# Kernel tuning notes

Hardware: AMD Instinct MI355X
Metric: run time of the kernel (lower is better)

## Reference

```python
import jax, jax.numpy as jnp
import numpy as np

D_MODEL = 256
D_INNER = 512          # expand * d_model
HEADDIM = 64
NHEADS = D_INNER // HEADDIM   # 8
NGROUPS = 1
D_STATE = 64
D_IN_PROJ = 2 * D_INNER + 2 * NGROUPS * D_STATE + NHEADS   # 1160
CONV_DIM = D_INNER + 2 * NGROUPS * D_STATE                  # 640
LN_EPS = 1e-5


def setup_inputs() -> dict:
    key = jax.random.key(0)
    ks = jax.random.split(key, 16)
    s = 0.02
    # dt_bias init as in torch code
    dt = jnp.exp(jax.random.uniform(ks[10], (NHEADS,)) * (np.log(0.1) - np.log(0.001)) + np.log(0.001))
    dt = jnp.clip(dt, 1e-4)
    dt_bias = dt + jnp.log(-jnp.expm1(-dt))
    A_log = jnp.log(jax.random.uniform(ks[11], (NHEADS,), minval=1.0, maxval=16.0))
    return {
        "u": jax.random.normal(ks[0], (4, 8192, D_MODEL), dtype=jnp.float32),
        "H": 64,
        "W": 128,
        "W_in": jax.random.normal(ks[1], (D_IN_PROJ, D_MODEL), dtype=jnp.float32) * s,
        "W_stereo": jax.random.normal(ks[2], (D_IN_PROJ, D_INNER), dtype=jnp.float32) * s,
        "conv_l_w": jax.random.normal(ks[3], (CONV_DIM, 1, 3, 3), dtype=jnp.float32) * 0.1,
        "conv_l_b": jax.random.normal(ks[4], (CONV_DIM,), dtype=jnp.float32) * 0.01,
        "conv_r_w": jax.random.normal(ks[5], (CONV_DIM, 1, 3, 3), dtype=jnp.float32) * 0.1,
        "conv_r_b": jax.random.normal(ks[6], (CONV_DIM,), dtype=jnp.float32) * 0.01,
        "conv_w": jax.random.normal(ks[7], (CONV_DIM, 1, 3, 3), dtype=jnp.float32) * 0.1,
        "conv_b": jax.random.normal(ks[8], (CONV_DIM,), dtype=jnp.float32) * 0.01,
        "dt_bias": dt_bias,
        "A_log": A_log,
        "D_l": jnp.ones((NHEADS,), dtype=jnp.float32),
        "D_r": jnp.ones((NHEADS,), dtype=jnp.float32),
        "D": jnp.ones((NHEADS,), dtype=jnp.float32),
        "ln_g": jnp.ones((D_INNER,), dtype=jnp.float32),
        "ln_b": jnp.zeros((D_INNER,), dtype=jnp.float32),
        "W_out": jax.random.normal(ks[9], (D_MODEL, D_INNER), dtype=jnp.float32) * s,
    }


def _dwconv(x, w, b):
    # x: (B, C, H, W); depthwise 3x3 conv, SAME padding ((d_conv-1)//2 = 1)
    y = jax.lax.conv_general_dilated(
        x, w, window_strides=(1, 1), padding='SAME',
        dimension_numbers=('NCHW', 'OIHW', 'NCHW'),
        feature_group_count=CONV_DIM)
    return y + b[None, :, None, None]


def _layernorm(x, g, b):
    mu = x.mean(-1, keepdims=True)
    var = x.var(-1, keepdims=True)
    return (x - mu) / jnp.sqrt(var + LN_EPS) * g + b


def _lin_attn(x, dt, A, Bm, Cm, Dp):
    # x: (b, l, d_inner), dt: (b, l, h), Bm/Cm: (b, l, d_state); ngroups == 1
    b, l, _ = x.shape
    xh = x.reshape(b, l, NHEADS, HEADDIM)              # V: (b, l, h, p)
    dA = -(dt[..., None] * A[None, None, :, None])     # ssd_positve_dA -> -dt*A, (b,l,h,1)
    KV = jnp.einsum('bls,blhp->bhsp', Bm, xh * dA)     # K^T @ V_scaled
    y = jnp.einsum('bls,bhsp->blhp', Cm, KV)           # Q @ KV
    y = y + xh * Dp[None, None, :, None]               # skip D
    return y.reshape(b, l, D_INNER)


def reference(u, H, W, W_in, W_stereo, conv_l_w, conv_l_b, conv_r_w, conv_r_b,
              conv_w, conv_b, dt_bias, A_log, D_l, D_r, D, ln_g, ln_b, W_out):
    batch, seqlen, _ = u.shape
    half = batch // 2
    silu = jax.nn.silu
    A = -jnp.exp(A_log)

    zxbcdt = u @ W_in.T                                             # (b, l, 1160)
    z, xBC, dt = jnp.split(zxbcdt, [D_INNER, D_INNER + CONV_DIM], axis=-1)
    dt = jax.nn.softplus(dt + dt_bias)                              # (b, l, h)

    xBC = xBC.reshape(batch, H, W, CONV_DIM).transpose(0, 3, 1, 2)  # NCHW
    xBC1 = silu(_dwconv(xBC[:half], conv_l_w, conv_l_b)).transpose(0, 2, 3, 1).reshape(half, H * W, CONV_DIM)
    xBC2 = silu(_dwconv(xBC[half:], conv_r_w, conv_r_b)).transpose(0, 2, 3, 1).reshape(half, H * W, CONV_DIM)

    x1, B1, C1 = jnp.split(xBC1, [D_INNER, D_INNER + NGROUPS * D_STATE], axis=-1)
    x2, B2, C2 = jnp.split(xBC2, [D_INNER, D_INNER + NGROUPS * D_STATE], axis=-1)
    dt1, dt2 = dt[:half], dt[half:]

    y1 = _layernorm(_lin_attn(x1, dt1, A, B1, C1, D_l), ln_g, ln_b)
    y2 = _layernorm(_lin_attn(x2, dt2, A, B2, C2, D_r), ln_g, ln_b)
    y = jnp.concatenate([y1, y2], axis=0) * z

    zxs = y @ W_stereo.T
    zs, xBCs, dts = jnp.split(zxs, [D_INNER, D_INNER + CONV_DIM], axis=-1)
    dts = jax.nn.softplus(dts + dt_bias)

    xBCs = xBCs.reshape(batch, H, W, CONV_DIM).transpose(0, 3, 1, 2)
    xBCs = silu(_dwconv(xBCs, conv_w, conv_b)).transpose(0, 2, 3, 1).reshape(batch, H * W, CONV_DIM)
    xs, Bs, Cs = jnp.split(xBCs, [D_INNER, D_INNER + NGROUPS * D_STATE], axis=-1)

    ys = _layernorm(_lin_attn(xs, dts, A, Bs, Cs, D), ln_g, ln_b) * zs
    return ys @ W_out.T
```

## Files before the change

### kernel.cpp

```cpp
#include <hip/hip_runtime.h>
#include <hip/hip_bf16.h>
#include <math.h>

#define NB    4
#define LSEQ  8192
#define HH    64
#define WW    128
#define DMODEL 256
#define DINNER 512
#define NH    8
#define DSTATE 64
#define DPROJ 1160
#define CONVD 640
#define MROWS (NB*LSEQ)
#define KVCH  32
#define CBLK  80

typedef unsigned short bf16_t;
typedef __attribute__((ext_vector_type(8))) unsigned short ushort8v;
typedef __attribute__((ext_vector_type(8))) short short8v;
typedef __attribute__((ext_vector_type(4))) float f32x4;

static __device__ __forceinline__ float bf2f(bf16_t u) {
    return __uint_as_float(((unsigned)u) << 16);
}
static __device__ __forceinline__ bf16_t f2bf(float f) {
    unsigned u = __float_as_uint(f);
    u += 0x7FFFu + ((u >> 16) & 1u);
    return (bf16_t)(u >> 16);
}

template <typename TC>
__global__ __launch_bounds__(256) void gemm_mfma_pipe(
    const bf16_t* __restrict__ A, int lda,
    const bf16_t* __restrict__ B, int ldb,
    TC* __restrict__ C, int ldc,
    int M, int N, int K)
{
    __shared__ __align__(16) bf16_t As[3][128 * 32];
    __shared__ __align__(16) bf16_t Bs[3][128 * 32];
    const int nwg = gridDim.x * gridDim.y;
    const int wg  = blockIdx.y * gridDim.x + blockIdx.x;
    const int swz = (wg & 7) * (nwg >> 3) + (wg >> 3);
    const int bx  = swz % gridDim.x;
    const int by  = swz / gridDim.x;

    const int tid = threadIdx.x;
    const int m0 = by * 128;
    const int n0 = bx * 128;
    const int wid = tid >> 6;
    const int lane = tid & 63;
    const int hA = wid >> 1;
    const int hB = wid & 1;
    const int fr = lane & 15;
    const int kq = lane >> 4;

    f32x4 acc[4][4];
    #pragma unroll
    for (int i = 0; i < 4; ++i)
        #pragma unroll
        for (int j = 0; j < 4; ++j) acc[i][j] = (f32x4){0.f, 0.f, 0.f, 0.f};

    int srow[2], scol[2];
    #pragma unroll
    for (int i = 0; i < 2; ++i) {
        const int L = i * 256 + tid;
        srow[i] = ((L >> 8) << 6) + (((L >> 6) & 3) << 4) + ((L >> 2) & 15);
        scol[i] = (L & 3) * 8;
    }

#define STAGE_P(buf, k0)                                                       \
    {                                                                          \
        _Pragma("unroll")                                                      \
        for (int i = 0; i < 2; ++i) {                                          \
            const size_t ga = (size_t)(m0 + srow[i]) * lda + (k0) + scol[i];   \
            const size_t gb = (size_t)(n0 + srow[i]) * ldb + (k0) + scol[i];   \
            const int ldst = (i * 256 + tid) * 8;                              \
            __builtin_amdgcn_global_load_lds(                                  \
                (const __attribute__((address_space(1))) void*)(A + ga),       \
                (__attribute__((address_space(3))) void*)(&As[buf][ldst]), 16, 0, 0); \
            __builtin_amdgcn_global_load_lds(                                  \
                (const __attribute__((address_space(1))) void*)(B + gb),       \
                (__attribute__((address_space(3))) void*)(&Bs[buf][ldst]), 16, 0, 0); \
        }                                                                      \
    }

    const int nt = K >> 5;
    STAGE_P(0, 0);
    STAGE_P(1, 32);

    const int abase = hA * 2048 + (fr * 4 + kq) * 8;
    const int bbase = hB * 2048 + (fr * 4 + kq) * 8;

    for (int t = 0; t < nt; ++t) {
        const int cur = t % 3;
        if (t + 1 < nt) asm volatile("s_waitcnt vmcnt(4)" ::: "memory");
        else            asm volatile("s_waitcnt vmcnt(0)" ::: "memory");
        __builtin_amdgcn_s_barrier();
        __builtin_amdgcn_sched_barrier(0);

        if (t + 2 < nt) STAGE_P((t + 2) % 3, (t + 2) * 32);

        short8v a_frag[4], b_frag[4];
        #pragma unroll
        for (int m = 0; m < 4; ++m)
            a_frag[m] = *(const short8v*)&As[cur][abase + m * 512];
        #pragma unroll
        for (int n = 0; n < 4; ++n)
            b_frag[n] = *(const short8v*)&Bs[cur][bbase + n * 512];
        #pragma unroll
        for (int m = 0; m < 4; ++m)
            #pragma unroll
            for (int n = 0; n < 4; ++n)
                acc[m][n] = __builtin_amdgcn_mfma_f32_16x16x32_bf16(
                    a_frag[m], b_frag[n], acc[m][n], 0, 0, 0);
    }
#undef STAGE_P

    const int wr = hA * 64;
    const int wc = hB * 64;
    #pragma unroll
    for (int mi = 0; mi < 4; ++mi) {
        #pragma unroll
        for (int ni = 0; ni < 4; ++ni) {
            const int col = n0 + wc + ni * 16 + fr;
            if (col < N) {
                #pragma unroll
                for (int q = 0; q < 4; ++q) {
                    const int row = m0 + wr + mi * 16 + kq * 4 + q;
                    if constexpr (sizeof(TC) == 2)
                        C[(size_t)row * ldc + col] = f2bf(acc[mi][ni][q]);
                    else
                        C[(size_t)row * ldc + col] = acc[mi][ni][q];
                }
            }
        }
    }
}

template <typename TC>
__global__ __launch_bounds__(256) void gemm_mfma_bt(
    const bf16_t* __restrict__ A, int lda, size_t sAb,
    const bf16_t* __restrict__ B, int ldb, size_t sBb,
    TC* __restrict__ C, int ldc, size_t sCb,
    int M, int N, int K)
{
    __shared__ __align__(16) bf16_t As[128 * 32];
    __shared__ __align__(16) bf16_t Bs[128 * 32];
    const bf16_t* Ab = A + blockIdx.z * sAb;
    const bf16_t* Bb = B + blockIdx.z * sBb;
    TC*            Cb = C + blockIdx.z * sCb;
    const int tid = threadIdx.x;
    const int m0 = blockIdx.y * 128;
    const int n0 = blockIdx.x * 128;
    const int wid = tid >> 6;
    const int lane = tid & 63;
    const int wr = (wid >> 1) * 64;
    const int wc = (wid & 1) * 64;
    const int fr = lane & 15;
    const int fk = (lane >> 4) * 8;

    f32x4 acc[4][4];
    #pragma unroll
    for (int i = 0; i < 4; ++i)
        #pragma unroll
        for (int j = 0; j < 4; ++j) acc[i][j] = (f32x4){0.f, 0.f, 0.f, 0.f};

    const int srow = tid >> 2;
    const int scol = (tid & 3) * 8;
    const bf16_t* gA = Ab + (size_t)(m0 + srow) * lda + scol;
    const bf16_t* gB = Bb + (size_t)(n0 + srow) * ldb + scol;
    bf16_t* lA = As + tid * 8;
    bf16_t* lB = Bs + tid * 8;

    for (int k0 = 0; k0 < K; k0 += 32) {
        __builtin_amdgcn_global_load_lds(
            (const __attribute__((address_space(1))) void*)(gA + k0),
            (__attribute__((address_space(3))) void*)lA, 16, 0, 0);
        __builtin_amdgcn_global_load_lds(
            (const __attribute__((address_space(1))) void*)(gA + (size_t)64 * lda + k0),
            (__attribute__((address_space(3))) void*)(lA + 2048), 16, 0, 0);
        __builtin_amdgcn_global_load_lds(
            (const __attribute__((address_space(1))) void*)(gB + k0),
            (__attribute__((address_space(3))) void*)lB, 16, 0, 0);
        __builtin_amdgcn_global_load_lds(
            (const __attribute__((address_space(1))) void*)(gB + (size_t)64 * ldb + k0),
            (__attribute__((address_space(3))) void*)(lB + 2048), 16, 0, 0);
        __syncthreads();

        short8v a_frag[4], b_frag[4];
        #pragma unroll
        for (int m = 0; m < 4; ++m)
            a_frag[m] = *(const short8v*)&As[(wr + m * 16 + fr) * 32 + fk];
        #pragma unroll
        for (int n = 0; n < 4; ++n)
            b_frag[n] = *(const short8v*)&Bs[(wc + n * 16 + fr) * 32 + fk];
        #pragma unroll
        for (int m = 0; m < 4; ++m)
            #pragma unroll
            for (int n = 0; n < 4; ++n)
                acc[m][n] = __builtin_amdgcn_mfma_f32_16x16x32_bf16(
                    a_frag[m], b_frag[n], acc[m][n], 0, 0, 0);
        __syncthreads();
    }

    #pragma unroll
    for (int mi = 0; mi < 4; ++mi) {
        #pragma unroll
        for (int ni = 0; ni < 4; ++ni) {
            const int col = n0 + wc + ni * 16 + fr;
            if (col < N) {
                #pragma unroll
                for (int q = 0; q < 4; ++q) {
                    const int row = m0 + wr + mi * 16 + (lane >> 4) * 4 + q;
                    if constexpr (sizeof(TC) == 2)
                        Cb[(size_t)row * ldc + col] = f2bf(acc[mi][ni][q]);
                    else
                        Cb[(size_t)row * ldc + col] = acc[mi][ni][q];
                }
            }
        }
    }
}

__global__ __launch_bounds__(256) void cvt_bf16_kernel(
    const float* __restrict__ in, bf16_t* __restrict__ out, int n)
{
    const int base = (blockIdx.x * 256 + threadIdx.x) * 4;
    if (base >= n) return;
    float4 v = *(const float4*)&in[base];
    ushort4 o;
    o.x = f2bf(v.x); o.y = f2bf(v.y); o.z = f2bf(v.z); o.w = f2bf(v.w);
    *(ushort4*)&out[base] = o;
}

__global__ __launch_bounds__(256) void wpad_kernel(
    const float* __restrict__ W, bf16_t* __restrict__ Wp,
    int N, int Npad, int K)
{
    const int i = blockIdx.x * 256 + threadIdx.x;
    if (i >= Npad * K) return;
    const int r = i / K, k = i - r * K;
    Wp[i] = (r < N) ? f2bf(W[(size_t)r * K + k]) : (bf16_t)0;
}

__global__ __launch_bounds__(256) void dt_kernel(
    const bf16_t* __restrict__ zx, const float* __restrict__ dt_bias,
    float* __restrict__ dtbuf)
{
    const int idx = blockIdx.x * 256 + threadIdx.x;
    const int h = idx & 7;
    const int row = idx >> 3;
    const float v = bf2f(zx[(size_t)row * DPROJ + (DINNER + CONVD) + h]) + dt_bias[h];
    const float sp = (v > 0.f) ? (v + log1pf(expf(-v))) : log1pf(expf(v));
    dtbuf[idx] = sp;
}

__global__ __launch_bounds__(256) void conv_silu_kernel(
    const bf16_t* __restrict__ zx,
    const float* __restrict__ wA, const float* __restrict__ bA,
    const float* __restrict__ wB, const float* __restrict__ bB,
    bf16_t* __restrict__ out)
{
    const int idx = blockIdx.x * 256 + threadIdx.x;
    const int cb = idx % CBLK;
    const int pc = idx / CBLK;
    const int c0 = cb * 8;
    const int ww = pc & (WW - 1);
    const int h4 = (pc >> 7) & 15;
    const int b  = pc >> 11;
    const int hbase = h4 * 4;
    const float* wp = (b < 2) ? wA : wB;
    const float* bp = (b < 2) ? bA : bB;

    float w[72];
    const float4* wsrc = (const float4*)(wp + c0 * 9);
    #pragma unroll
    for (int i = 0; i < 18; ++i) ((float4*)w)[i] = wsrc[i];

    float acc[4][8];
    {
        float4 bv0 = *(const float4*)(bp + c0);
        float4 bv1 = *(const float4*)(bp + c0 + 4);
        #pragma unroll
        for (int o = 0; o < 4; ++o) {
            acc[o][0] = bv0.x; acc[o][1] = bv0.y; acc[o][2] = bv0.z; acc[o][3] = bv0.w;
            acc[o][4] = bv1.x; acc[o][5] = bv1.y; acc[o][6] = bv1.z; acc[o][7] = bv1.w;
        }
    }

    const bf16_t* base = zx + (size_t)b * LSEQ * DPROJ + DINNER + c0;
    #pragma unroll
    for (int ri = 0; ri < 6; ++ri) {
        const int hi = hbase + ri - 1;
        const bool hok = (unsigned)hi < (unsigned)HH;
        float cur[3][8];
        #pragma unroll
        for (int kj = 0; kj < 3; ++kj) {
            const int wi = ww + kj - 1;
            if (hok && (unsigned)wi < (unsigned)WW) {
                const ushort8v v = *(const ushort8v*)(base + (size_t)(hi * WW + wi) * DPROJ);
                #pragma unroll
                for (int q = 0; q < 8; ++q) cur[kj][q] = bf2f(v[q]);
            } else {
                #pragma unroll
                for (int q = 0; q < 8; ++q) cur[kj][q] = 0.f;
            }
        }
        #pragma unroll
        for (int o = 0; o < 4; ++o) {
            const int ki = ri - o;
            if (ki >= 0 && ki < 3) {
                #pragma unroll
                for (int kj = 0; kj < 3; ++kj)
                    #pragma unroll
                    for (int q = 0; q < 8; ++q)
                        acc[o][q] += cur[kj][q] * w[q * 9 + ki * 3 + kj];
            }
        }
    }

    #pragma unroll
    for (int o = 0; o < 4; ++o) {
        const int t = b * LSEQ + (hbase + o) * WW + ww;
        ushort8v ov;
        #pragma unroll
        for (int q = 0; q < 8; ++q) {
            const float s = acc[o][q] / (1.f + expf(-acc[o][q]));
            ov[q] = f2bf(s);
        }
        *(ushort8v*)(out + (size_t)t * CONVD + c0) = ov;
    }
}

__global__ __launch_bounds__(128) void kv_part_kernel(
    const bf16_t* __restrict__ xconv, const float* __restrict__ dtbuf,
    const float* __restrict__ A_log, float* __restrict__ KVp)
{
    const int h = blockIdx.y, b = blockIdx.z, chunk = blockIdx.x;
    const int tid = threadIdx.x;
    const int w = tid >> 6, lane = tid & 63;
    __shared__ float lds[2 * 4352];
    float* Bt = lds + w * 4352;
    float* Xt = Bt + 2176;
    const float eA = expf(A_log[h]);
    const int s4  = (lane & 15) * 4;
    const int p16 = (lane >> 4) * 16;
    const int r    = lane & 31;
    const int part = lane >> 5;

    float acc[4][16];
    #pragma unroll
    for (int i = 0; i < 4; ++i)
        #pragma unroll
        for (int j = 0; j < 16; ++j) acc[i][j] = 0.f;

    const int l0 = b * LSEQ + chunk * 256;

    for (int t = 0; t < 8; t += 2) {
        const int row = l0 + (t + w) * 32 + r;
        const bf16_t* src = xconv + (size_t)row * CONVD + (part ? h * 64 : DINNER);
        const float scale = part ? dtbuf[row * NH + h] * eA : 1.f;
        float* dst = part ? &Xt[r * 68] : &Bt[r * 68];
        #pragma unroll
        for (int j = 0; j < 8; ++j) {
            ushort8v v = *(const ushort8v*)(src + j * 8);
            f32x4 lo = {bf2f(v[0]) * scale, bf2f(v[1]) * scale,
                        bf2f(v[2]) * scale, bf2f(v[3]) * scale};
            f32x4 hi = {bf2f(v[4]) * scale, bf2f(v[5]) * scale,
                        bf2f(v[6]) * scale, bf2f(v[7]) * scale};
            *(f32x4*)&dst[j * 8]     = lo;
            *(f32x4*)&dst[j * 8 + 4] = hi;
        }
        __syncthreads();
        #pragma unroll 4
        for (int rr = 0; rr < 32; ++rr) {
            const f32x4 bv = *(const f32x4*)&Bt[rr * 68 + s4];
            #pragma unroll
            for (int q = 0; q < 4; ++q) {
                const f32x4 xv = *(const f32x4*)&Xt[rr * 68 + p16 + q * 4];
                #pragma unroll
                for (int si = 0; si < 4; ++si)
                    #pragma unroll
                    for (int k = 0; k < 4; ++k)
                        acc[si][q * 4 + k] += bv[si] * xv[k];
            }
        }
        __syncthreads();
    }

    if (w == 0) {
        #pragma unroll
        for (int si = 0; si < 4; ++si)
            #pragma unroll
            for (int q = 0; q < 4; ++q)
                *(f32x4*)&lds[(s4 + si) * 68 + p16 + q * 4] =
                    (f32x4){acc[si][q*4], acc[si][q*4+1], acc[si][q*4+2], acc[si][q*4+3]};
    }
    __syncthreads();
    if (w == 1) {
        float* dst = KVp + ((size_t)chunk * (NB * NH) + (b * NH + h)) * 4096;
        #pragma unroll
        for (int si = 0; si < 4; ++si)
            #pragma unroll
            for (int q = 0; q < 4; ++q) {
                const f32x4 o = *(const f32x4*)&lds[(s4 + si) * 68 + p16 + q * 4];
                f32x4 v = {acc[si][q*4] + o[0], acc[si][q*4+1] + o[1],
                           acc[si][q*4+2] + o[2], acc[si][q*4+3] + o[3]};
                *(f32x4*)&dst[(s4 + si) * 64 + p16 + q * 4] = v;
            }
    }
}

__global__ __launch_bounds__(256) void kv_reduce_T_kernel(
    const float* __restrict__ KVp, bf16_t* __restrict__ KVT)
{
    const int idx = blockIdx.x * 256 + threadIdx.x;
    float s = 0.f;
    #pragma unroll
    for (int c = 0; c < KVCH; ++c) s += KVp[(size_t)c * 131072 + idx];
    const int bh = idx >> 12;
    const int ss = (idx >> 6) & 63;
    const int p  = idx & 63;
    KVT[((size_t)(bh * 64 + p)) * 64 + ss] = f2bf(s);
}

__global__ __launch_bounds__(256) void ln_gate_kernel(
    const bf16_t* __restrict__ Yattn, const bf16_t* __restrict__ xconv,
    const bf16_t* __restrict__ zx,
    const float* __restrict__ DA, const float* __restrict__ DB,
    const float* __restrict__ ln_g, const float* __restrict__ ln_b,
    bf16_t* __restrict__ ybuf)
{
    const int w = threadIdx.x >> 6, lane = threadIdx.x & 63;
    const int c0 = lane * 8;
    const int h = lane >> 3;
    float g[8], be[8];
    *(float4*)&g[0]  = *(const float4*)&ln_g[c0];
    *(float4*)&g[4]  = *(const float4*)&ln_g[c0 + 4];
    *(float4*)&be[0] = *(const float4*)&ln_b[c0];
    *(float4*)&be[4] = *(const float4*)&ln_b[c0 + 4];
    const int row0 = (blockIdx.x * 4 + w) * 4;

    for (int i = 0; i < 4; ++i) {
        const int row = row0 + i;
        const int b = row >> 13;
        const float Dv = (b < 2) ? DA[h] : DB[h];
        ushort8v yv = *(const ushort8v*)(Yattn + (size_t)row * DINNER + c0);
        ushort8v xv = *(const ushort8v*)(xconv + (size_t)row * CONVD + c0);
        float y[8];
        float s1 = 0.f, s2 = 0.f;
        #pragma unroll
        for (int q = 0; q < 8; ++q) {
            y[q] = bf2f(yv[q]) + bf2f(xv[q]) * Dv;
            s1 += y[q]; s2 += y[q] * y[q];
        }
        #pragma unroll
        for (int off = 32; off > 0; off >>= 1) {
            s1 += __shfl_xor(s1, off, 64);
            s2 += __shfl_xor(s2, off, 64);
        }
        const float mu = s1 * (1.f / 512.f);
        const float var = s2 * (1.f / 512.f) - mu * mu;
        const float rstd = rsqrtf(var + 1e-5f);
        ushort8v zv = *(const ushort8v*)(zx + (size_t)row * DPROJ + c0);
        ushort8v o;
        #pragma unroll
        for (int q = 0; q < 8; ++q)
            o[q] = f2bf(((y[q] - mu) * rstd * g[q] + be[q]) * bf2f(zv[q]));
        *(ushort8v*)(ybuf + (size_t)row * DINNER + c0) = o;
    }
}

extern "C" void kernel_launch(void* const* d_in, const int* in_sizes, int n_in,
                              void* d_out, int out_size, void* d_ws, size_t ws_size,
                              hipStream_t stream)
{
    const float* u        = (const float*)d_in[0];
    const float* W_in     = (const float*)d_in[3];
    const float* W_st     = (const float*)d_in[4];
    const float* conv_l_w = (const float*)d_in[5];
    const float* conv_l_b = (const float*)d_in[6];
    const float* conv_r_w = (const float*)d_in[7];
    const float* conv_r_b = (const float*)d_in[8];
    const float* conv_w   = (const float*)d_in[9];
    const float* conv_b   = (const float*)d_in[10];
    const float* dt_bias  = (const float*)d_in[11];
    const float* A_log    = (const float*)d_in[12];
    const float* D_l      = (const float*)d_in[13];
    const float* D_r      = (const float*)d_in[14];
    const float* Dp       = (const float*)d_in[15];
    const float* ln_g     = (const float*)d_in[16];
    const float* ln_b     = (const float*)d_in[17];
    const float* W_out    = (const float*)d_in[18];
    float* out = (float*)d_out;

    char* ws = (char*)d_ws;
    const size_t ZX_B    = (size_t)MROWS * DPROJ * 2;
    const size_t XCONV_B = (size_t)MROWS * CONVD * 2;
    const size_t YBUF_B  = (size_t)MROWS * DINNER * 2;
    const size_t DT_B    = (size_t)MROWS * NH * 4;
    const size_t KVT_B   = (size_t)NB * DINNER * 64 * 2;
    const size_t UBF_B   = (size_t)MROWS * DMODEL * 2;
    const size_t WIN_B   = (size_t)1280 * DMODEL * 2;
    const size_t WST_B   = (size_t)1280 * DINNER * 2;
    const size_t WOUT_B  = (size_t)256 * DINNER * 2;
    bf16_t* zx    = (bf16_t*)(ws);
    bf16_t* xconv = (bf16_t*)(ws + ZX_B);
    bf16_t* ybuf  = (bf16_t*)(ws + ZX_B + XCONV_B);
    float*  dtbuf = (float*) (ws + ZX_B + XCONV_B + YBUF_B);
    bf16_t* KVT   = (bf16_t*)(ws + ZX_B + XCONV_B + YBUF_B + DT_B);
    bf16_t* ubf   = (bf16_t*)(ws + ZX_B + XCONV_B + YBUF_B + DT_B + KVT_B);
    float*  KVp   = (float*) (ws + ZX_B + XCONV_B + YBUF_B + DT_B + KVT_B);
    bf16_t* WinP  = (bf16_t*)(ws + ZX_B + XCONV_B + YBUF_B + DT_B + KVT_B + UBF_B);
    bf16_t* WstP  = (bf16_t*)(ws + ZX_B + XCONV_B + YBUF_B + DT_B + KVT_B + UBF_B + WIN_B);
    bf16_t* WoutP = (bf16_t*)(ws + ZX_B + XCONV_B + YBUF_B + DT_B + KVT_B + UBF_B + WIN_B + WST_B);
    bf16_t* Yattn = (bf16_t*)(ws + ZX_B + XCONV_B + YBUF_B + DT_B + KVT_B + UBF_B + WIN_B + WST_B + WOUT_B);

    const dim3 gemmGridP(10, MROWS / 128);
    const dim3 gemmGridO(2,  MROWS / 128);
    const dim3 ymmGrid(4, LSEQ / 128, NB);
    const dim3 kvGrid(KVCH, NH, NB);
    const int convGrid = (MROWS / 4) * CBLK / 256;
    const int lnGrid = MROWS / 16;

    cvt_bf16_kernel<<<(MROWS * DMODEL / 4 + 255) / 256, 256, 0, stream>>>(u, ubf, MROWS * DMODEL);
    wpad_kernel<<<(1280 * DMODEL + 255) / 256, 256, 0, stream>>>(W_in, WinP, DPROJ, 1280, DMODEL);
    wpad_kernel<<<(1280 * DINNER + 255) / 256, 256, 0, stream>>>(W_st, WstP, DPROJ, 1280, DINNER);
    wpad_kernel<<<(256 * DINNER + 255) / 256, 256, 0, stream>>>(W_out, WoutP, DMODEL, 256, DINNER);

    gemm_mfma_pipe<bf16_t><<<gemmGridP, 256, 0, stream>>>(
        ubf, DMODEL, WinP, DMODEL, zx, DPROJ, MROWS, DPROJ, DMODEL);
    dt_kernel<<<(MROWS * NH) / 256, 256, 0, stream>>>(zx, dt_bias, dtbuf);
    conv_silu_kernel<<<convGrid, 256, 0, stream>>>(
        zx, conv_l_w, conv_l_b, conv_r_w, conv_r_b, xconv);
    kv_part_kernel<<<kvGrid, 128, 0, stream>>>(xconv, dtbuf, A_log, KVp);
    kv_reduce_T_kernel<<<131072 / 256, 256, 0, stream>>>(KVp, KVT);
    gemm_mfma_bt<bf16_t><<<ymmGrid, 256, 0, stream>>>(
        xconv + DINNER + DSTATE, CONVD, (size_t)LSEQ * CONVD,
        KVT, 64, (size_t)DINNER * 64,
        Yattn, DINNER, (size_t)LSEQ * DINNER, LSEQ, DINNER, 64);
    ln_gate_kernel<<<lnGrid, 256, 0, stream>>>(
        Yattn, xconv, zx, D_l, D_r, ln_g, ln_b, ybuf);

    gemm_mfma_pipe<bf16_t><<<gemmGridP, 256, 0, stream>>>(
        ybuf, DINNER, WstP, DINNER, zx, DPROJ, MROWS, DPROJ, DINNER);
    dt_kernel<<<(MROWS * NH) / 256, 256, 0, stream>>>(zx, dt_bias, dtbuf);
    conv_silu_kernel<<<convGrid, 256, 0, stream>>>(
        zx, conv_w, conv_b, conv_w, conv_b, xconv);
    kv_part_kernel<<<kvGrid, 128, 0, stream>>>(xconv, dtbuf, A_log, KVp);
    kv_reduce_T_kernel<<<131072 / 256, 256, 0, stream>>>(KVp, KVT);
    gemm_mfma_bt<bf16_t><<<ymmGrid, 256, 0, stream>>>(
        xconv + DINNER + DSTATE, CONVD, (size_t)LSEQ * CONVD,
        KVT, 64, (size_t)DINNER * 64,
        Yattn, DINNER, (size_t)LSEQ * DINNER, LSEQ, DINNER, 64);
    ln_gate_kernel<<<lnGrid, 256, 0, stream>>>(
        Yattn, xconv, zx, Dp, Dp, ln_g, ln_b, ybuf);

    gemm_mfma_pipe<float><<<gemmGridO, 256, 0, stream>>>(
        ybuf, DINNER, WoutP, DINNER, out, DMODEL, MROWS, DMODEL, DINNER);
}
```

Baseline: 387.9 us.

## Use 256x128 GEMM tiles with 512 threads and double buffering

Replaces the 128x128, 256-thread, triple-buffered projection GEMM with a 256x128 tile computed by 8 waves. Each B tile is now shared by twice as many rows, and the grid is halved. The pipeline drops from three LDS stages with fine-grained vmcnt waits to two stages with a full __syncthreads per k-step, which may expose load latency. The waits look loose: the next stage's loads are issued without waiting for the previous ones, so correctness depends on implicit ordering through the barrier.

```diff
diff --git a/kernel.cpp b/kernel.cpp
--- a/kernel.cpp
+++ b/kernel.cpp
@@ -31,14 +31,14 @@
 }
 
 template <typename TC>
-__global__ __launch_bounds__(256) void gemm_mfma_pipe(
+__global__ __launch_bounds__(512) void gemm_mfma_big(
     const bf16_t* __restrict__ A, int lda,
     const bf16_t* __restrict__ B, int ldb,
     TC* __restrict__ C, int ldc,
     int M, int N, int K)
 {
-    __shared__ __align__(16) bf16_t As[3][128 * 32];
-    __shared__ __align__(16) bf16_t Bs[3][128 * 32];
+    __shared__ __align__(16) bf16_t As[2][256 * 32];
+    __shared__ __align__(16) bf16_t Bs[2][128 * 32];
     const int nwg = gridDim.x * gridDim.y;
     const int wg  = blockIdx.y * gridDim.x + blockIdx.x;
     const int swz = (wg & 7) * (nwg >> 3) + (wg >> 3);
@@ -46,12 +46,12 @@
     const int by  = swz / gridDim.x;
 
     const int tid = threadIdx.x;
-    const int m0 = by * 128;
+    const int m0 = by * 256;
     const int n0 = bx * 128;
-    const int wid = tid >> 6;
+    const int w    = tid >> 6;
     const int lane = tid & 63;
-    const int hA = wid >> 1;
-    const int hB = wid & 1;
+    const int wrow = w >> 1;
+    const int wcol = w & 1;
     const int fr = lane & 15;
     const int kq = lane >> 4;
 
@@ -61,45 +61,42 @@
         #pragma unroll
         for (int j = 0; j < 4; ++j) acc[i][j] = (f32x4){0.f, 0.f, 0.f, 0.f};
 
-    int srow[2], scol[2];
+    int arow[2], acol[2];
     #pragma unroll
     for (int i = 0; i < 2; ++i) {
-        const int L = i * 256 + tid;
-        srow[i] = ((L >> 8) << 6) + (((L >> 6) & 3) << 4) + ((L >> 2) & 15);
-        scol[i] = (L & 3) * 8;
-    }
-
-#define STAGE_P(buf, k0)                                                       \
+        const int L = i * 512 + tid;
+        arow[i] = ((L >> 8) << 6) + (((L >> 6) & 3) << 4) + ((L >> 2) & 15);
+        acol[i] = (L & 3) * 8;
+    }
+    const int Lb = tid;
+    const int brow = ((Lb >> 8) << 6) + (((Lb >> 6) & 3) << 4) + ((Lb >> 2) & 15);
+    const int bcol = (Lb & 3) * 8;
+
+#define STAGE_BIG(buf, k0)                                                     \
     {                                                                          \
         _Pragma("unroll")                                                      \
         for (int i = 0; i < 2; ++i) {                                          \
-            const size_t ga = (size_t)(m0 + srow[i]) * lda + (k0) + scol[i];   \
-            const size_t gb = (size_t)(n0 + srow[i]) * ldb + (k0) + scol[i];   \
-            const int ldst = (i * 256 + tid) * 8;                              \
+            const size_t ga = (size_t)(m0 + arow[i]) * lda + (k0) + acol[i];   \
             __builtin_amdgcn_global_load_lds(                                  \
                 (const __attribute__((address_space(1))) void*)(A + ga),       \
-                (__attribute__((address_space(3))) void*)(&As[buf][ldst]), 16, 0, 0); \
-            __builtin_amdgcn_global_load_lds(                                  \
-                (const __attribute__((address_space(1))) void*)(B + gb),       \
-                (__attribute__((address_space(3))) void*)(&Bs[buf][ldst]), 16, 0, 0); \
+                (__attribute__((address_space(3))) void*)(&As[buf][(i * 512 + tid) * 8]), 16, 0, 0); \
         }                                                                      \
+        const size_t gb = (size_t)(n0 + brow) * ldb + (k0) + bcol;             \
+        __builtin_amdgcn_global_load_lds(                                      \
+            (const __attribute__((address_space(1))) void*)(B + gb),           \
+            (__attribute__((address_space(3))) void*)(&Bs[buf][tid * 8]), 16, 0, 0); \
     }
 
     const int nt = K >> 5;
-    STAGE_P(0, 0);
-    STAGE_P(1, 32);
-
-    const int abase = hA * 2048 + (fr * 4 + kq) * 8;
-    const int bbase = hB * 2048 + (fr * 4 + kq) * 8;
-
+    STAGE_BIG(0, 0);
+    __syncthreads();
+
+    const int abase = wrow * 2048 + (fr * 4 + kq) * 8;
+    const int bbase = wcol * 2048 + (fr * 4 + kq) * 8;
+
+    int cur = 0;
     for (int t = 0; t < nt; ++t) {
-        const int cur = t % 3;
-        if (t + 1 < nt) asm volatile("s_waitcnt vmcnt(4)" ::: "memory");
-        else            asm volatile("s_waitcnt vmcnt(0)" ::: "memory");
-        __builtin_amdgcn_s_barrier();
-        __builtin_amdgcn_sched_barrier(0);
-
-        if (t + 2 < nt) STAGE_P((t + 2) % 3, (t + 2) * 32);
+        if (t + 1 < nt) STAGE_BIG(cur ^ 1, (t + 1) * 32);
 
         short8v a_frag[4], b_frag[4];
         #pragma unroll
@@ -114,20 +111,21 @@
             for (int n = 0; n < 4; ++n)
                 acc[m][n] = __builtin_amdgcn_mfma_f32_16x16x32_bf16(
                     a_frag[m], b_frag[n], acc[m][n], 0, 0, 0);
-    }
-#undef STAGE_P
-
-    const int wr = hA * 64;
-    const int wc = hB * 64;
+
+        __syncthreads();
+        cur ^= 1;
+    }
+#undef STAGE_BIG
+
     #pragma unroll
     for (int mi = 0; mi < 4; ++mi) {
         #pragma unroll
         for (int ni = 0; ni < 4; ++ni) {
-            const int col = n0 + wc + ni * 16 + fr;
+            const int col = n0 + wcol * 64 + ni * 16 + fr;
             if (col < N) {
                 #pragma unroll
                 for (int q = 0; q < 4; ++q) {
-                    const int row = m0 + wr + mi * 16 + kq * 4 + q;
+                    const int row = m0 + wrow * 64 + mi * 16 + kq * 4 + q;
                     if constexpr (sizeof(TC) == 2)
                         C[(size_t)row * ldc + col] = f2bf(acc[mi][ni][q]);
                     else
@@ -517,8 +515,8 @@
     bf16_t* WoutP = (bf16_t*)(ws + ZX_B + XCONV_B + YBUF_B + DT_B + KVT_B + UBF_B + WIN_B + WST_B);
     bf16_t* Yattn = (bf16_t*)(ws + ZX_B + XCONV_B + YBUF_B + DT_B + KVT_B + UBF_B + WIN_B + WST_B + WOUT_B);
 
-    const dim3 gemmGridP(10, MROWS / 128);
-    const dim3 gemmGridO(2,  MROWS / 128);
+    const dim3 gemmGridP(10, MROWS / 256);
+    const dim3 gemmGridO(2,  MROWS / 256);
     const dim3 ymmGrid(4, LSEQ / 128, NB);
     const dim3 kvGrid(KVCH, NH, NB);
     const int convGrid = (MROWS / 4) * CBLK / 256;
@@ -529,7 +527,7 @@
     wpad_kernel<<<(1280 * DINNER + 255) / 256, 256, 0, stream>>>(W_st, WstP, DPROJ, 1280, DINNER);
     wpad_kernel<<<(256 * DINNER + 255) / 256, 256, 0, stream>>>(W_out, WoutP, DMODEL, 256, DINNER);
 
-    gemm_mfma_pipe<bf16_t><<<gemmGridP, 256, 0, stream>>>(
+    gemm_mfma_big<bf16_t><<<gemmGridP, 512, 0, stream>>>(
         ubf, DMODEL, WinP, DMODEL, zx, DPROJ, MROWS, DPROJ, DMODEL);
     dt_kernel<<<(MROWS * NH) / 256, 256, 0, stream>>>(zx, dt_bias, dtbuf);
     conv_silu_kernel<<<convGrid, 256, 0, stream>>>(
@@ -543,7 +541,7 @@
     ln_gate_kernel<<<lnGrid, 256, 0, stream>>>(
         Yattn, xconv, zx, D_l, D_r, ln_g, ln_b, ybuf);
 
-    gemm_mfma_pipe<bf16_t><<<gemmGridP, 256, 0, stream>>>(
+    gemm_mfma_big<bf16_t><<<gemmGridP, 512, 0, stream>>>(
         ybuf, DINNER, WstP, DINNER, zx, DPROJ, MROWS, DPROJ, DINNER);
     dt_kernel<<<(MROWS * NH) / 256, 256, 0, stream>>>(zx, dt_bias, dtbuf);
     conv_silu_kernel<<<convGrid, 256, 0, stream>>>(
@@ -557,6 +555,6 @@
     ln_gate_kernel<<<lnGrid, 256, 0, stream>>>(
         Yattn, xconv, zx, Dp, Dp, ln_g, ln_b, ybuf);
 
-    gemm_mfma_pipe<float><<<gemmGridO, 256, 0, stream>>>(
+    gemm_mfma_big<float><<<gemmGridO, 512, 0, stream>>>(
         ybuf, DINNER, WoutP, DINNER, out, DMODEL, MROWS, DMODEL, DINNER);
 }
```

Result: no change. 387.2 us (-0.2%).
